# Kernel tuning notes

Measured on AMD Instinct MI355X. Metric: run time of the kernel, lower is better.

## Reference

```python
import jax, jax.numpy as jnp
import numpy as np

N_EMBD = 768
HEAD_SIZE = 64
B, T = 32, 1024


def setup_inputs() -> dict:
    key = jax.random.key(0)
    k1, k2, k3, k4 = jax.random.split(key, 4)
    x = jax.random.normal(k1, (B, T, N_EMBD), dtype=jnp.float32)
    Wq = jax.random.normal(k2, (N_EMBD, HEAD_SIZE), dtype=jnp.float32) * 0.02
    Wk = jax.random.normal(k3, (N_EMBD, HEAD_SIZE), dtype=jnp.float32) * 0.02
    Wv = jax.random.normal(k4, (N_EMBD, HEAD_SIZE), dtype=jnp.float32) * 0.02
    return {"x": x, "Wq": Wq, "Wk": Wk, "Wv": Wv}


def _apply_rope(q, k):
    # q, k: [B, T, D]; interleaved (even/odd) RoPE exactly as the torch source
    seq_len, dim = q.shape[-2], q.shape[-1]
    pos = jnp.arange(seq_len, dtype=jnp.float32)[:, None]                      # [T, 1]
    div_term = jnp.exp(jnp.arange(0, dim, 2, dtype=jnp.float32) * (-jnp.log(10000.0) / dim))  # [D/2]
    sin_emb = jnp.sin(pos * div_term)                                          # [T, D/2]
    cos_emb = jnp.cos(pos * div_term)                                          # [T, D/2]

    def rot(t):
        te, to = t[..., ::2], t[..., 1::2]
        re = te * cos_emb - to * sin_emb
        ro = te * sin_emb + to * cos_emb
        # interleave back: [..., T, D/2, 2] -> [..., T, D]
        return jnp.stack([re, ro], axis=-1).reshape(t.shape)

    return rot(q), rot(k)


def reference(x, Wq, Wk, Wv):
    Bx, Tx, C = x.shape  # C == n_embd
    q = x @ Wq  # [B, T, D]
    k = x @ Wk
    v = x @ Wv
    q, k = _apply_rope(q, k)
    # NOTE: source scales by C**-0.5 where C = n_embd, not head_size
    wei = jnp.einsum('btd,bsd->bts', q, k) * (C ** -0.5)  # [B, T, T]
    causal = jnp.tril(jnp.ones((Tx, Tx), dtype=bool))
    wei = jnp.where(causal, wei, -jnp.inf)
    wei = jax.nn.softmax(wei, axis=-1)
    # dropout is identity in eval mode
    out = jnp.einsum('bts,bsd->btd', wei, v)  # [B, T, D]
    return out
```

## Files before the change

kernel.cpp:

```cpp
#include <hip/hip_runtime.h>
#include <cmath>

#define B 32
#define T 1024
#define CDIM 768
#define D 64
#define SCALE 0.03608439182435161f
#define XSTR 72

typedef short bf16x8 __attribute__((ext_vector_type(8)));
typedef float f32x4 __attribute__((ext_vector_type(4)));
typedef float f32x16 __attribute__((ext_vector_type(16)));
typedef unsigned short u16x8 __attribute__((ext_vector_type(8)));

__device__ inline ushort f2bf(float f) {
  union { float f; unsigned u; } v{f};
  unsigned r = (v.u + 0x7FFFu + ((v.u >> 16) & 1u)) >> 16;
  return (ushort)r;
}

__global__ __launch_bounds__(256) void wt_prep(
    const float* __restrict__ Wq, const float* __restrict__ Wk,
    const float* __restrict__ Wv, ushort* __restrict__ Wt)
{
  const int n   = blockIdx.x;
  const int sel = n >> 6, col = n & 63;
  const float* W = (sel == 0) ? Wq : (sel == 1) ? Wk : Wv;
  const float sc = (sel == 0) ? SCALE : 1.f;
  for (int k = threadIdx.x; k < CDIM; k += 256)
    Wt[(size_t)n * CDIM + k] = f2bf(W[(size_t)k * D + col] * sc);
}

__global__ __launch_bounds__(256) void proj_mfma(
    const float* __restrict__ x,
    const ushort* __restrict__ Wt,
    ushort* __restrict__ qkv)
{
  const int t    = threadIdx.x;
  const int lane = t & 63;
  const int wid  = t >> 6;
  const int ln32 = lane & 31;
  const int half = lane >> 5;
  const int mw   = wid & 1;
  const int nh   = wid >> 1;
  const int row0 = blockIdx.x * 64;

  __shared__ ushort Xs[2][64 * XSTR];
  __shared__ ushort Ws[2][192 * XSTR];

  f32x16 acc[3];
  #pragma unroll
  for (int nt = 0; nt < 3; ++nt)
    #pragma unroll
    for (int rg = 0; rg < 16; ++rg) acc[nt][rg] = 0.f;

  float4 xp[2][4];
  u16x8  wp[2][6];

  auto load_stage = [&](int s, int set) {
    const int k0 = s * 64;
    #pragma unroll
    for (int it = 0; it < 4; ++it) {
      int slot = it * 256 + t, row = slot >> 4, kq = slot & 15;
      xp[set][it] = *(const float4*)(x + (size_t)(row0 + row) * CDIM + k0 + kq * 4);
    }
    #pragma unroll
    for (int it = 0; it < 6; ++it) {
      int slot = it * 256 + t, n = slot >> 3, kb = slot & 7;
      wp[set][it] = *(const u16x8*)(Wt + (size_t)n * CDIM + k0 + kb * 8);
    }
  };

  load_stage(0, 0);
  load_stage(1, 1);
  int buf = 0;
  for (int s = 0; s < CDIM / 64; ++s) {
    const int set = s & 1;
    #pragma unroll
    for (int it = 0; it < 4; ++it) {
      int slot = it * 256 + t, row = slot >> 4, kq = slot & 15;
      ushort4 bv;
      bv.x = f2bf(xp[set][it].x); bv.y = f2bf(xp[set][it].y);
      bv.z = f2bf(xp[set][it].z); bv.w = f2bf(xp[set][it].w);
      *(ushort4*)&Xs[buf][row * XSTR + kq * 4] = bv;
    }
    #pragma unroll
    for (int it = 0; it < 6; ++it) {
      int slot = it * 256 + t, n = slot >> 3, kb = slot & 7;
      *(u16x8*)&Ws[buf][n * XSTR + kb * 8] = wp[set][it];
    }
    __syncthreads();
    if (s + 2 < CDIM / 64) load_stage(s + 2, set);

    #pragma unroll
    for (int kk = 0; kk < 4; ++kk) {
      bf16x8 a = *(const bf16x8*)&Xs[buf][(mw * 32 + ln32) * XSTR + kk * 16 + half * 8];
      #pragma unroll
      for (int nt = 0; nt < 3; ++nt) {
        bf16x8 bb = *(const bf16x8*)&Ws[buf][(nh * 96 + nt * 32 + ln32) * XSTR + kk * 16 + half * 8];
        acc[nt] = __builtin_amdgcn_mfma_f32_32x32x16_bf16(a, bb, acc[nt], 0, 0, 0);
      }
    }
    buf ^= 1;
  }

  #pragma unroll
  for (int nt = 0; nt < 3; ++nt) {
    const int n   = nh * 96 + nt * 32 + ln32;
    const int sel = n >> 6;
    const int d   = n & 63;
    ushort* outb = qkv + (size_t)sel * (B * T * D);
    if (sel < 2) {
      const float freq = __expf((float)(d & 62) * (-0.14391156855801f));
      const float sgn  = (d & 1) ? 1.f : -1.f;
      #pragma unroll
      for (int reg = 0; reg < 16; ++reg) {
        int rowg = row0 + mw * 32 + (reg & 3) + 8 * (reg >> 2) + 4 * half;
        float sv, cv;
        __sincosf((float)(rowg & (T - 1)) * freq, &sv, &cv);
        float val = acc[nt][reg];
        float partner = __shfl_xor(val, 1, 64);
        outb[(size_t)rowg * D + d] = f2bf(fmaf(sgn * partner, sv, val * cv));
      }
    } else {
      #pragma unroll
      for (int reg = 0; reg < 16; ++reg) {
        int rowg = row0 + mw * 32 + (reg & 3) + 8 * (reg >> 2) + 4 * half;
        outb[(size_t)rowg * D + d] = f2bf(acc[nt][reg]);
      }
    }
  }
}

__global__ __launch_bounds__(256) void attn_mfma(
    const ushort* __restrict__ qg,
    const ushort* __restrict__ kg,
    const ushort* __restrict__ vg,
    float* __restrict__ out)
{
  const int t    = threadIdx.x;
  const int lane = t & 63;
  const int wid  = t >> 6;
  const int ln16 = lane & 15;
  const int quad = lane >> 4;
  const int l    = (int)blockIdx.x;
  const int b    = l & 31;
  const int r    = l >> 5;
  const int qt   = (r < 8) ? r : 23 - r;

  __shared__ ushort Ks[2][64 * XSTR];
  __shared__ ushort Vt[2][64 * XSTR];
  __shared__ ushort Pl[64 * XSTR];

  bf16x8 qf[2];
  {
    const ushort* qrow = qg + (size_t)(b * T + qt * 64 + wid * 16 + ln16) * D;
    qf[0] = *(const bf16x8*)(qrow + quad * 8);
    qf[1] = *(const bf16x8*)(qrow + quad * 8 + 32);
  }

  f32x4 O[4];
  #pragma unroll
  for (int nt = 0; nt < 4; ++nt) O[nt] = (f32x4){0.f, 0.f, 0.f, 0.f};
  float l_sum = 0.f;

  const int kb = t & 15, db = t >> 4;
  const int d0 = db * 4, kk0 = kb * 4;

  u16x8  kp[2];
  ushort4 vp[4];
  auto load_kv = [&](int kt) {
    #pragma unroll
    for (int i = 0; i < 2; ++i) {
      int slot = i * 256 + t, row = slot >> 3, dblk = slot & 7;
      kp[i] = *(const u16x8*)(kg + (size_t)(b * T + kt * 64 + row) * D + dblk * 8);
    }
    #pragma unroll
    for (int i = 0; i < 4; ++i)
      vp[i] = *(const ushort4*)(vg + (size_t)(b * T + kt * 64 + kk0 + i) * D + d0);
  };

  load_kv(0);
  int buf = 0;
  for (int kt = 0; kt <= qt; ++kt) {
    #pragma unroll
    for (int i = 0; i < 2; ++i) {
      int slot = i * 256 + t, row = slot >> 3, dblk = slot & 7;
      *(u16x8*)&Ks[buf][row * XSTR + dblk * 8] = kp[i];
    }
    const ushort* vpe = (const ushort*)vp;
    #pragma unroll
    for (int j = 0; j < 4; ++j) {
      ushort4 c;
      c.x = vpe[0 * 4 + j]; c.y = vpe[1 * 4 + j];
      c.z = vpe[2 * 4 + j]; c.w = vpe[3 * 4 + j];
      *(ushort4*)&Vt[buf][(d0 + j) * XSTR + kk0] = c;
    }
    __syncthreads();
    if (kt < qt) load_kv(kt + 1);

    f32x4 s[4];
    #pragma unroll
    for (int mt = 0; mt < 4; ++mt) s[mt] = (f32x4){0.f, 0.f, 0.f, 0.f};
    #pragma unroll
    for (int ks = 0; ks < 2; ++ks)
      #pragma unroll
      for (int mt = 0; mt < 4; ++mt) {
        bf16x8 kf = *(const bf16x8*)&Ks[buf][(mt * 16 + ln16) * XSTR + quad * 8 + ks * 32];
        s[mt] = __builtin_amdgcn_mfma_f32_16x16x32_bf16(kf, qf[ks], s[mt], 0, 0, 0);
      }

    if (kt == qt) {
      const int ql = wid * 16 + ln16;
      #pragma unroll
      for (int mt = 0; mt < 4; ++mt)
        #pragma unroll
        for (int reg = 0; reg < 4; ++reg)
          if (mt * 16 + quad * 4 + reg > ql) s[mt][reg] = -1e30f;
    }

    float psum = 0.f;
    #pragma unroll
    for (int mt = 0; mt < 4; ++mt) {
      float p0 = __expf(s[mt][0]), p1 = __expf(s[mt][1]);
      float p2 = __expf(s[mt][2]), p3 = __expf(s[mt][3]);
      psum += (p0 + p1) + (p2 + p3);
      ushort4 pk;
      pk.x = f2bf(p0); pk.y = f2bf(p1); pk.z = f2bf(p2); pk.w = f2bf(p3);
      *(ushort4*)&Pl[(wid * 16 + ln16) * XSTR + mt * 16 + quad * 4] = pk;
    }
    psum += __shfl_xor(psum, 16, 64);
    psum += __shfl_xor(psum, 32, 64);
    l_sum += psum;

    bf16x8 pa[2];
    pa[0] = *(const bf16x8*)&Pl[(wid * 16 + ln16) * XSTR + quad * 8];
    pa[1] = *(const bf16x8*)&Pl[(wid * 16 + ln16) * XSTR + quad * 8 + 32];
    #pragma unroll
    for (int ks = 0; ks < 2; ++ks)
      #pragma unroll
      for (int nt = 0; nt < 4; ++nt) {
        bf16x8 vf = *(const bf16x8*)&Vt[buf][(nt * 16 + ln16) * XSTR + quad * 8 + ks * 32];
        O[nt] = __builtin_amdgcn_mfma_f32_16x16x32_bf16(pa[ks], vf, O[nt], 0, 0, 0);
      }
    buf ^= 1;
  }

  float inv = 1.f / l_sum;
  #pragma unroll
  for (int reg = 0; reg < 4; ++reg) {
    float iv = __shfl(inv, quad * 4 + reg, 64);
    size_t row = (size_t)(b * T + qt * 64 + wid * 16 + quad * 4 + reg) * D;
    #pragma unroll
    for (int nt = 0; nt < 4; ++nt)
      out[row + nt * 16 + ln16] = O[nt][reg] * iv;
  }
}

extern "C" void kernel_launch(void* const* d_in, const int* in_sizes, int n_in,
                              void* d_out, int out_size, void* d_ws, size_t ws_size,
                              hipStream_t stream) {
  const float* x  = (const float*)d_in[0];
  const float* Wq = (const float*)d_in[1];
  const float* Wk = (const float*)d_in[2];
  const float* Wv = (const float*)d_in[3];
  float* outp = (float*)d_out;

  ushort* qkv = (ushort*)d_ws;
  ushort* Wt  = qkv + (size_t)3 * B * T * D;

  wt_prep<<<dim3(192), dim3(256), 0, stream>>>(Wq, Wk, Wv, Wt);
  proj_mfma<<<dim3((B * T) / 64), dim3(256), 0, stream>>>(x, Wt, qkv);
  attn_mfma<<<dim3(T / 64 * B), dim3(256), 0, stream>>>(
      qkv, qkv + (size_t)B * T * D, qkv + 2 * (size_t)B * T * D, outp);
}
```

Measured before the change: 181.1 us.

## Stage projection operands via direct global-to-LDS loads with swizzled layouts

The projection kernel now uses global_load_lds to copy x (as fp32) and the pre-tiled weights straight into shared memory, with XOR swizzles in place of padded strides. Weight prep writes Wt in a per-stage, swizzled layout so each stage is one contiguous block. The fp32 to bf16 conversion of x moves from the store path to the point where fragments are read from LDS. This removes the register staging and per-thread LDS writes, but the weight buffer is now single-buffered behind explicit vmcnt waits and two barriers per stage, and the conversion is redone for each MFMA fragment read.

Result: no change. 182.6 us (+0.9%).

```diff
diff --git a/kernel.cpp b/kernel.cpp
--- a/kernel.cpp
+++ b/kernel.cpp
@@ -17,6 +17,12 @@
   union { float f; unsigned u; } v{f};
   unsigned r = (v.u + 0x7FFFu + ((v.u >> 16) & 1u)) >> 16;
   return (ushort)r;
+}
+
+__device__ __forceinline__ void gll16(const void* g, void* l) {
+  __builtin_amdgcn_global_load_lds(
+      (const __attribute__((address_space(1))) void*)g,
+      (__attribute__((address_space(3))) void*)l, 16, 0, 0);
 }
 
 __global__ __launch_bounds__(256) void wt_prep(
@@ -27,8 +33,11 @@
   const int sel = n >> 6, col = n & 63;
   const float* W = (sel == 0) ? Wq : (sel == 1) ? Wk : Wv;
   const float sc = (sel == 0) ? SCALE : 1.f;
-  for (int k = threadIdx.x; k < CDIM; k += 256)
-    Wt[(size_t)n * CDIM + k] = f2bf(W[(size_t)k * D + col] * sc);
+  const int swz = (n & 7) << 3;
+  for (int k = threadIdx.x; k < CDIM; k += 256) {
+    const int s = k >> 6, kl = k & 63;
+    Wt[(size_t)(s * 192 + n) * 64 + (kl ^ swz)] = f2bf(W[(size_t)k * D + col] * sc);
+  }
 }
 
 __global__ __launch_bounds__(256) void proj_mfma(
@@ -45,8 +54,8 @@
   const int nh   = wid >> 1;
   const int row0 = blockIdx.x * 64;
 
-  __shared__ ushort Xs[2][64 * XSTR];
-  __shared__ ushort Ws[2][192 * XSTR];
+  __shared__ float  Xf[2][64 * 64];
+  __shared__ ushort Wl[192 * 64];
 
   f32x16 acc[3];
   #pragma unroll
@@ -54,54 +63,62 @@
     #pragma unroll
     for (int rg = 0; rg < 16; ++rg) acc[nt][rg] = 0.f;
 
-  float4 xp[2][4];
-  u16x8  wp[2][6];
-
-  auto load_stage = [&](int s, int set) {
-    const int k0 = s * 64;
-    #pragma unroll
-    for (int it = 0; it < 4; ++it) {
-      int slot = it * 256 + t, row = slot >> 4, kq = slot & 15;
-      xp[set][it] = *(const float4*)(x + (size_t)(row0 + row) * CDIM + k0 + kq * 4);
-    }
-    #pragma unroll
-    for (int it = 0; it < 6; ++it) {
-      int slot = it * 256 + t, n = slot >> 3, kb = slot & 7;
-      wp[set][it] = *(const u16x8*)(Wt + (size_t)n * CDIM + k0 + kb * 8);
+  const float* xb0 = x + (size_t)row0 * CDIM;
+
+  auto stage_X = [&](int s, int bu) {
+    #pragma unroll
+    for (int i = 0; i < 4; ++i) {
+      const int lin = i * 256 + wid * 64 + lane;
+      const int row = lin >> 4, sl = lin & 15;
+      const int c   = sl ^ (row & 15);
+      gll16(xb0 + (size_t)row * CDIM + s * 64 + c * 4,
+            &Xf[bu][(i * 256 + wid * 64) * 4]);
     }
   };
-
-  load_stage(0, 0);
-  load_stage(1, 1);
-  int buf = 0;
+  auto stage_W = [&](int s) {
+    const ushort* wb = Wt + (size_t)s * (192 * 64);
+    #pragma unroll
+    for (int i = 0; i < 6; ++i) {
+      const int lin = i * 256 + wid * 64 + lane;
+      gll16(wb + lin * 8, &Wl[(i * 256 + wid * 64) * 8]);
+    }
+  };
+
+  const int xr  = mw * 32 + ln32;
+  const int xsw = xr & 15;
+
+  stage_X(0, 0);
+  #pragma unroll
   for (int s = 0; s < CDIM / 64; ++s) {
-    const int set = s & 1;
-    #pragma unroll
-    for (int it = 0; it < 4; ++it) {
-      int slot = it * 256 + t, row = slot >> 4, kq = slot & 15;
-      ushort4 bv;
-      bv.x = f2bf(xp[set][it].x); bv.y = f2bf(xp[set][it].y);
-      bv.z = f2bf(xp[set][it].z); bv.w = f2bf(xp[set][it].w);
-      *(ushort4*)&Xs[buf][row * XSTR + kq * 4] = bv;
-    }
-    #pragma unroll
-    for (int it = 0; it < 6; ++it) {
-      int slot = it * 256 + t, n = slot >> 3, kb = slot & 7;
-      *(u16x8*)&Ws[buf][n * XSTR + kb * 8] = wp[set][it];
-    }
-    __syncthreads();
-    if (s + 2 < CDIM / 64) load_stage(s + 2, set);
+    const int bu = s & 1;
+    stage_W(s);
+    if (s + 1 < CDIM / 64) {
+      stage_X(s + 1, bu ^ 1);
+      asm volatile("s_waitcnt vmcnt(4)" ::: "memory");
+    } else {
+      asm volatile("s_waitcnt vmcnt(0)" ::: "memory");
+    }
+    __builtin_amdgcn_s_barrier();
 
     #pragma unroll
     for (int kk = 0; kk < 4; ++kk) {
-      bf16x8 a = *(const bf16x8*)&Xs[buf][(mw * 32 + ln32) * XSTR + kk * 16 + half * 8];
+      const int c0 = kk * 4 + half * 2;
+      f32x4 f0 = *(const f32x4*)&Xf[bu][xr * 64 + ((c0 ^ xsw) << 2)];
+      f32x4 f1 = *(const f32x4*)&Xf[bu][xr * 64 + (((c0 + 1) ^ xsw) << 2)];
+      union { ushort u[8]; bf16x8 v; } af;
+      af.u[0] = f2bf(f0[0]); af.u[1] = f2bf(f0[1]);
+      af.u[2] = f2bf(f0[2]); af.u[3] = f2bf(f0[3]);
+      af.u[4] = f2bf(f1[0]); af.u[5] = f2bf(f1[1]);
+      af.u[6] = f2bf(f1[2]); af.u[7] = f2bf(f1[3]);
       #pragma unroll
       for (int nt = 0; nt < 3; ++nt) {
-        bf16x8 bb = *(const bf16x8*)&Ws[buf][(nh * 96 + nt * 32 + ln32) * XSTR + kk * 16 + half * 8];
-        acc[nt] = __builtin_amdgcn_mfma_f32_32x32x16_bf16(a, bb, acc[nt], 0, 0, 0);
-      }
-    }
-    buf ^= 1;
+        const int wr = nh * 96 + nt * 32 + ln32;
+        const int cc = (kk * 2 + half) ^ (wr & 7);
+        bf16x8 bb = *(const bf16x8*)&Wl[wr * 64 + (cc << 3)];
+        acc[nt] = __builtin_amdgcn_mfma_f32_32x32x16_bf16(af.v, bb, acc[nt], 0, 0, 0);
+      }
+    }
+    __builtin_amdgcn_s_barrier();
   }
 
   #pragma unroll
```
